# Kernel tuning notes

Hardware: AMD Instinct MI355X
Metric: run time of the kernel (lower is better)

Reference implementation:

```python
import jax, jax.numpy as jnp
import numpy as np

N, D = 1024, 8          # total neurons, neuron_size
I, O = 64, 64           # input / output layer sizes
HN = N - I - O          # hidden layer size (896)
TICKS = 2
DIN = 2 * D + 1         # GRU input: [pre, post, reward]


def setup_inputs() -> dict:
    key = jax.random.key(0)
    ks = jax.random.split(key, 40)

    def rn(k, shape, s=1.0):
        return jax.random.normal(k, shape, jnp.float32) * s

    # Bernoulli(0.5) adjacency + structural validation (as in vallidate_Adjacency_matrix)
    A = np.array(jax.random.uniform(ks[2], (N, N)) < 0.5, dtype=np.int32)
    A[:I, :I] = 0
    A[:I, N - O:] = 0
    A[I:I + HN, :I] = 0
    A[N - O:, :I] = 0
    A[N - O:, N - O:] = 0
    if A[:I].sum() == 0:
        A[0, I] = 1

    inp = {
        'obs': rn(ks[0], (I,)),
        'reward': rn(ks[1], (1,)),
        'adjacency': jnp.asarray(A),
        'hidden0': rn(ks[3], (N, N, D)),
        'post0': rn(ks[4], (N, D)),
        'lr': jnp.full((1,), 0.01, jnp.float32),
    }
    s = 1.0 / np.sqrt(D)
    i = 5
    for pre in ('fc_in', 'fc_hid', 'fc_out'):
        inp[pre + '_w'] = rn(ks[i], (D, D), s); i += 1
        inp[pre + '_b'] = rn(ks[i], (D,), s); i += 1
    for pre in ('gin', 'ghid', 'gout'):
        inp[pre + '_wih'] = rn(ks[i], (3 * D, DIN), s); i += 1
        inp[pre + '_whh'] = rn(ks[i], (3 * D, D), s); i += 1
        inp[pre + '_bih'] = rn(ks[i], (3 * D,), s); i += 1
        inp[pre + '_bhh'] = rn(ks[i], (3 * D,), s); i += 1
    return inp


def _gru(x, h, wih, whh, bih, bhh):
    # torch.nn.GRUCell math
    gx = x @ wih.T + bih          # (..., 3D)
    gh = h @ whh.T + bhh
    xr, xz, xn = jnp.split(gx, 3, axis=-1)
    hr, hz, hn = jnp.split(gh, 3, axis=-1)
    r = jax.nn.sigmoid(xr + hr)
    z = jax.nn.sigmoid(xz + hz)
    n = jnp.tanh(xn + r * hn)
    return (1.0 - z) * n + z * h


def _forward(obs, reward, adjacency, hidden0, post0, lr,
             fc_in_w, fc_in_b, fc_hid_w, fc_hid_b, fc_out_w, fc_out_b,
             gin_wih, gin_whh, gin_bih, gin_bhh,
             ghid_wih, ghid_whh, ghid_bih, ghid_bhh,
             gout_wih, gout_whh, gout_bih, gout_bhh):
    def syn(pre_rows, P, H_read, wih, whh, bih, bhh):
        # dense-masked edge update over an (L, N) layer slice; same math as the
        # per-edge GRUCell, computed for all pairs then masked on write.
        L = pre_rows.shape[0]
        pre = jnp.broadcast_to(pre_rows[:, None, :], (L, N, D))
        post = jnp.broadcast_to(P[None, :, :], (L, N, D))
        rew = jnp.broadcast_to(reward.reshape(1, 1, 1), (L, N, 1))
        x = jnp.concatenate([pre, post, rew], axis=-1)   # (L, N, 2D+1)
        g = _gru(x, H_read, wih, whh, bih, bhh)
        upd = H_read + g * lr
        return upd * pre, upd

    m_in = (adjacency[:I] == 1)[..., None]           # (I, N, 1)
    m_hid = (adjacency[I:I + HN] == 1)[..., None]    # (HN, N, 1)
    m_out = (adjacency[N - O:] == 1)[..., None]      # (O, N, 1)

    inp_sig = jnp.broadcast_to(obs[:, None], (I, D))
    H, P = hidden0, post0
    PH = jnp.zeros((N, N, D), jnp.float32)           # placeholder (persists across ticks)

    for _ in range(TICKS):
        # input layer neurons + synapses (writes rows [:I])
        P = P.at[:I].set(jnp.tanh(inp_sig @ fc_in_w.T + fc_in_b))
        out, upd = syn(P[:I], P, H[:I], gin_wih, gin_whh, gin_bih, gin_bhh)
        PH = PH.at[:I].set(jnp.where(m_in, out, PH[:I]))
        H = H.at[:I].set(jnp.where(m_in, upd, H[:I]))

        # hidden layer neurons + synapses
        P = P.at[I:I + HN].set(jnp.tanh(PH[:, I:I + HN].sum(axis=0) @ fc_hid_w.T + fc_hid_b))
        out, upd = syn(P[I:I + HN], P, H[I:I + HN], ghid_wih, ghid_whh, ghid_bih, ghid_bhh)
        # NOTE: the torch code reads hidden rows offset by I but WRITES unshifted
        # rows [:HN] of both placeholder and hidden_state; replicated faithfully.
        PH = PH.at[:HN].set(jnp.where(m_hid, out, PH[:HN]))
        H = H.at[:HN].set(jnp.where(m_hid, upd, H[:HN]))

        # output layer neurons + synapses
        P = P.at[N - O:].set(jnp.tanh(PH[:, N - O:].sum(axis=0) @ fc_out_w.T + fc_out_b))
        out, upd = syn(P[N - O:], P, H[I + HN:], gout_wih, gout_whh, gout_bih, gout_bhh)
        # torch reads hidden rows offset by I+HN but writes unshifted rows [:O]
        PH = PH.at[:O].set(jnp.where(m_out, out, PH[:O]))
        H = H.at[:O].set(jnp.where(m_out, upd, H[:O]))

    return P


def reference(obs, reward, adjacency, hidden0, post0, lr,
              fc_in_w, fc_in_b, fc_hid_w, fc_hid_b, fc_out_w, fc_out_b,
              gin_wih, gin_whh, gin_bih, gin_bhh,
              ghid_wih, ghid_whh, ghid_bih, ghid_bhh,
              gout_wih, gout_whh, gout_bih, gout_bhh):
    P = _forward(obs, reward, adjacency, hidden0, post0, lr,
                 fc_in_w, fc_in_b, fc_hid_w, fc_hid_b, fc_out_w, fc_out_b,
                 gin_wih, gin_whh, gin_bih, gin_bhh,
                 ghid_wih, ghid_whh, ghid_bih, ghid_bhh,
                 gout_wih, gout_whh, gout_bih, gout_bhh)
    return jnp.argmax(P[N - O:, 0])
```

## Files before the change

kernel.cpp:

```cpp
#include <hip/hip_runtime.h>

#define NN 1024

typedef float f32x8 __attribute__((ext_vector_type(8)));


__device__ __forceinline__ float sigmoid_f(float x)
{
    return __fdividef(1.f, 1.f + __expf(-x));
}
__device__ __forceinline__ float tanh_f(float x)
{
    float ax = fabsf(x);
    float e  = __expf(-2.f * ax);
    float t  = __fdividef(1.f - e, 1.f + e);
    return copysignf(t, x);
}
__device__ __forceinline__ f32x8 ld8(const float* __restrict__ p) { return *(const f32x8*)p; }
__device__ __forceinline__ void st8(float* __restrict__ p, f32x8 v) { *(f32x8*)p = v; }

__device__ __forceinline__ f32x8 gru_core(const float (*__restrict__ sWH)[8],
                                          const float* __restrict__ sGX,
                                          const float* __restrict__ sBhh,
                                          const float* __restrict__ gxp,
                                          f32x8 h, float lr)
{
    f32x8 gr = ld8(gxp), gz = ld8(gxp + 8), gn = ld8(gxp + 16);
    f32x8 upd;
#pragma unroll
    for (int d = 0; d < 8; ++d) {
        float hr = sBhh[d], hz = sBhh[8 + d], hn = sBhh[16 + d];
#pragma unroll
        for (int k = 0; k < 8; ++k) {
            hr = fmaf(sWH[d][k],      h[k], hr);
            hz = fmaf(sWH[8 + d][k],  h[k], hz);
            hn = fmaf(sWH[16 + d][k], h[k], hn);
        }
        float r  = sigmoid_f(sGX[d] + gr[d] + hr);
        float z  = sigmoid_f(sGX[8 + d] + gz[d] + hz);
        float nv = tanh_f(fmaf(r, hn, sGX[16 + d] + gn[d]));
        float g  = (1.f - z) * nv + z * h[d];
        upd[d] = fmaf(g, lr, h[d]);
    }
    return upd;
}

#define SYN_STAGE(PREROW)                                                               \
    __shared__ float sWH[24][8]; __shared__ float sGX[24]; __shared__ float sBhh[24];   \
    { int t_ = threadIdx.x;                                                             \
      if (t_ < 192) { int j = t_ >> 3, k = t_ & 7; sWH[j][k] = Whh[j * 8 + k]; }        \
      else if (t_ < 216) { int j = t_ - 192;                                            \
        float a = Bih[j] + Wih[j * 17 + 16] * reward[0];                                \
        _Pragma("unroll") for (int k = 0; k < 8; ++k)                                   \
            a = fmaf(Wih[j * 17 + k], P[(PREROW) * 8 + k], a);                          \
        sGX[j] = a; sBhh[j] = Bhh[j]; }                                                 \
      __syncthreads(); }

__global__ void __launch_bounds__(256)
k_prep(const float* __restrict__ obs, const float* __restrict__ fiw,
       const float* __restrict__ fib, const float* __restrict__ post0,
       float* __restrict__ P, float* __restrict__ GXPin1, float* __restrict__ GXPhid1,
       const float* __restrict__ gin_wih, const float* __restrict__ ghid_wih)
{
    int t = threadIdx.x, b = blockIdx.x;
    int gid = b * 256 + t;
    float pv;
    if (gid < 512) {
        int i = gid >> 3, j = gid & 7;
        float rs = 0.f;
#pragma unroll
        for (int d = 0; d < 8; ++d) rs += fiw[j * 8 + d];
        pv = tanhf(obs[i] * rs + fib[j]);
    } else {
        pv = post0[gid];
    }
    P[gid] = pv;
    __shared__ float sP[256];
    sP[t] = pv;
    __syncthreads();
    int c0 = b * 32;
    const float* W = nullptr; float* dst = nullptr;
    if (c0 >= 64 && c0 < 960) { W = gin_wih;  dst = GXPin1; }
    else if (c0 >= 960)       { W = ghid_wih; dst = GXPhid1; }
    if (dst) {
        for (int v = t; v < 768; v += 256) {
            int c = v / 24, j = v % 24;
            float a = 0.f;
#pragma unroll
            for (int k = 0; k < 8; ++k) a = fmaf(W[j * 17 + 8 + k], sP[c * 8 + k], a);
            dst[(c0 + c) * 24 + j] = a;
        }
    }
}

template <int TICK>
__global__ void __launch_bounds__(256, 4)
k_syn_in(const int* __restrict__ A, const float* __restrict__ hidden0,
         const float* __restrict__ P, float* __restrict__ PH,
         float* __restrict__ Uin, const float* __restrict__ Utop,
         const float* __restrict__ Uout, const float* __restrict__ GXP,
         const float* __restrict__ Wih, const float* __restrict__ Whh,
         const float* __restrict__ Bih, const float* __restrict__ Bhh,
         const float* __restrict__ reward, const float* __restrict__ lr)
{
    int r = blockIdx.x >> 2;
    SYN_STAGE(r);
    int n = 64 + ((blockIdx.x & 3) << 8) + threadIdx.x;
    if (n >= NN) return;
    int e = (r * NN + n) * 8;
    if (!A[r * NN + n]) {
        if (TICK == 1) { f32x8 z{}; st8(PH + e, z); }
        return;
    }
    f32x8 h;
    if (TICK == 1) {
        h = ld8(hidden0 + e);
    } else {
        const float* src = Uin + e;
        if (A[(960 + r) * NN + n])     src = Uout + e;
        else if (A[(64 + r) * NN + n]) src = Utop + e;
        h = ld8(src);
    }
    f32x8 upd = gru_core(sWH, sGX, sBhh, GXP + n * 24, h, lr[0]);
    f32x8 pre = ld8(P + r * 8);
    st8(PH + e, upd * pre);
    if (TICK == 1) st8(Uin + e, upd);
}

__global__ void __launch_bounds__(256, 4)
k_syn_hid1(const int* __restrict__ A, const float* __restrict__ hidden0,
           const float* __restrict__ P, float* __restrict__ PH,
           float* __restrict__ Utop, float* __restrict__ Urt,
           const float* __restrict__ GXP,
           const float* __restrict__ Wih, const float* __restrict__ Whh,
           const float* __restrict__ Bih, const float* __restrict__ Bhh,
           const float* __restrict__ reward, const float* __restrict__ lr)
{
    int l = blockIdx.x >> 2;
    SYN_STAGE(64 + l);
    int n = 64 + ((blockIdx.x & 3) << 8) + threadIdx.x;
    if (n >= NN) return;
    int e = (l * NN + n) * 8;
    if (!A[(64 + l) * NN + n]) {
        if (l >= 64) { f32x8 z{}; st8(PH + e, z); }
        return;
    }
    f32x8 h = ld8(hidden0 + ((64 + l) * NN + n) * 8);
    f32x8 upd = gru_core(sWH, sGX, sBhh, GXP + n * 24, h, lr[0]);
    f32x8 pre = ld8(P + (64 + l) * 8);
    st8(PH + e, upd * pre);
    if (l < 64) st8(Utop + e, upd);
    if (n >= 960) st8(Urt + (l * 64 + (n - 960)) * 8, upd);
}

__global__ void __launch_bounds__(256, 4)
k_syn_out(const int* __restrict__ A, const float* __restrict__ hidden0,
          const float* __restrict__ P, float* __restrict__ PH,
          float* __restrict__ Uout, const float* __restrict__ GXP,
          const float* __restrict__ Wih, const float* __restrict__ Whh,
          const float* __restrict__ Bih, const float* __restrict__ Bhh,
          const float* __restrict__ reward, const float* __restrict__ lr)
{
    int l = blockIdx.x >> 2;
    SYN_STAGE(960 + l);
    int n = 64 + ((blockIdx.x & 3) << 8) + threadIdx.x;
    if (n >= NN) return;
    if (!A[(960 + l) * NN + n]) return;
    f32x8 h = ld8(hidden0 + ((960 + l) * NN + n) * 8);
    f32x8 upd = gru_core(sWH, sGX, sBhh, GXP + n * 24, h, lr[0]);
    f32x8 pre = ld8(P + (960 + l) * 8);
    int e = (l * NN + n) * 8;
    st8(PH + e, upd * pre);
    st8(Uout + e, upd);
}

__global__ void __launch_bounds__(256, 4)
k_syn_hid2(const int* __restrict__ A, const float* __restrict__ hidden0,
           const float* __restrict__ P, float* __restrict__ PH,
           const float* __restrict__ Urt, const float* __restrict__ GXP,
           const float* __restrict__ Wih, const float* __restrict__ Whh,
           const float* __restrict__ Bih, const float* __restrict__ Bhh,
           const float* __restrict__ reward, const float* __restrict__ lr)
{
    __shared__ float sWH[24][8]; __shared__ float sBhh[24]; __shared__ float sGX4[4][24];
    int t = threadIdx.x;
    if (t < 192) { int j = t >> 3, k = t & 7; sWH[j][k] = Whh[j * 8 + k]; }
    else if (t < 216) sBhh[t - 192] = Bhh[t - 192];
    if (t < 96) {
        int rr = t / 24, j = t % 24;
        int l = blockIdx.x * 4 + rr;
        float a = Bih[j] + Wih[j * 17 + 16] * reward[0];
#pragma unroll
        for (int k = 0; k < 8; ++k) a = fmaf(Wih[j * 17 + k], P[(64 + l) * 8 + k], a);
        sGX4[rr][j] = a;
    }
    __syncthreads();
    int rr = t >> 6, nn = t & 63;
    int l = blockIdx.x * 4 + rr, n = 960 + nn;
    if (!A[(64 + l) * NN + n]) return;
    const float* hp = (l < 832 && A[(128 + l) * NN + n]) ? (Urt + ((64 + l) * 64 + nn) * 8)
                                                         : (hidden0 + ((64 + l) * NN + n) * 8);
    f32x8 h = ld8(hp);
    f32x8 upd = gru_core(sWH, sGX4[rr], sBhh, GXP + n * 24, h, lr[0]);
    f32x8 pre = ld8(P + (64 + l) * 8);
    st8(PH + (l * NN + n) * 8, upd * pre);
}

__global__ void __launch_bounds__(256)
k_sum_hid1(const float* __restrict__ PH, float* __restrict__ P,
           const float* __restrict__ W, const float* __restrict__ b,
           float* __restrict__ GXPhid1, float* __restrict__ GXPout,
           float* __restrict__ GXPin2,
           const float* __restrict__ ghid_wih, const float* __restrict__ gout_wih,
           const float* __restrict__ gin_wih)
{
    int t = threadIdx.x;
    int c0 = 64 + blockIdx.x * 32;
    int base = c0 * 8 + t;
    float acc = 0.f;
    for (int r = 0; r < 64; ++r) acc += PH[r * 8192 + base];
    __shared__ float sS[256];
    sS[t] = acc; __syncthreads();
    int j = t & 7;
    float z = b[j];
#pragma unroll
    for (int d = 0; d < 8; ++d) z = fmaf(sS[(t & ~7) | d], W[j * 8 + d], z);
    float pv = tanhf(z);
    P[base] = pv;
    __shared__ float sP[256];
    sP[t] = pv; __syncthreads();
    for (int v = t; v < 768; v += 256) {
        int c = v / 24, jj = v % 24;
        float a1 = 0.f, a2 = 0.f, a3 = 0.f;
#pragma unroll
        for (int k = 0; k < 8; ++k) {
            float p = sP[c * 8 + k];
            a1 = fmaf(ghid_wih[jj * 17 + 8 + k], p, a1);
            a2 = fmaf(gout_wih[jj * 17 + 8 + k], p, a2);
            a3 = fmaf(gin_wih [jj * 17 + 8 + k], p, a3);
        }
        int o = (c0 + c) * 24 + jj;
        GXPhid1[o] = a1; GXPout[o] = a2; GXPin2[o] = a3;
    }
}

template <bool DO_GXP>
__global__ void __launch_bounds__(512)
k_sumN(const float* __restrict__ PH, float* __restrict__ P,
       const float* __restrict__ W, const float* __restrict__ b,
       int col0, float* __restrict__ GXPdst, const float* __restrict__ gWih)
{
    int t = threadIdx.x;
    int col = (t >> 3) & 7, dim = t & 7, chunk = t >> 6;
    int gc0 = col0 + blockIdx.x * 8;
    float acc = 0.f;
    int base = (gc0 + col) * 8 + dim;
    for (int r = chunk * 112; r < chunk * 112 + 112; ++r) acc += PH[r * 8192 + base];
    __shared__ float sA[8][64];
    sA[chunk][(col << 3) | dim] = acc;
    __syncthreads();
    __shared__ float sS[64];
    if (t < 64) {
        float s = 0.f;
#pragma unroll
        for (int c = 0; c < 8; ++c) s += sA[c][t];
        sS[t] = s;
    }
    __syncthreads();
    __shared__ float sPn[64];
    if (t < 64) {
        int cl = t >> 3, j = t & 7;
        float z = b[j];
#pragma unroll
        for (int d = 0; d < 8; ++d) z = fmaf(sS[(cl << 3) | d], W[j * 8 + d], z);
        float pv = tanhf(z);
        P[(gc0 + cl) * 8 + j] = pv;
        sPn[t] = pv;
    }
    __syncthreads();
    if (DO_GXP && t < 192) {
        int c = t / 24, j = t % 24;
        float a = 0.f;
#pragma unroll
        for (int k = 0; k < 8; ++k) a = fmaf(gWih[j * 17 + 8 + k], sPn[c * 8 + k], a);
        GXPdst[(gc0 + c) * 24 + j] = a;
    }
}

__global__ void __launch_bounds__(64)
k_argmax(const float* __restrict__ P, float* __restrict__ out)
{
    __shared__ float v[64];
    int t = threadIdx.x;
    v[t] = P[(960 + t) * 8];
    __syncthreads();
    if (t == 0) {
        int best = 0; float bv = v[0];
        for (int j = 1; j < 64; ++j)
            if (v[j] > bv) { bv = v[j]; best = j; }
        out[0] = (float)best;
    }
}

extern "C" void kernel_launch(void* const* d_in, const int* in_sizes, int n_in,
                              void* d_out, int out_size, void* d_ws, size_t ws_size,
                              hipStream_t stream)
{
    const float* obs      = (const float*)d_in[0];
    const float* reward   = (const float*)d_in[1];
    const int*   A        = (const int*)d_in[2];
    const float* hidden0  = (const float*)d_in[3];
    const float* post0    = (const float*)d_in[4];
    const float* lr       = (const float*)d_in[5];
    const float* fc_in_w  = (const float*)d_in[6];
    const float* fc_in_b  = (const float*)d_in[7];
    const float* fc_hid_w = (const float*)d_in[8];
    const float* fc_hid_b = (const float*)d_in[9];
    const float* fc_out_w = (const float*)d_in[10];
    const float* fc_out_b = (const float*)d_in[11];
    const float* gin_wih  = (const float*)d_in[12];
    const float* gin_whh  = (const float*)d_in[13];
    const float* gin_bih  = (const float*)d_in[14];
    const float* gin_bhh  = (const float*)d_in[15];
    const float* ghid_wih = (const float*)d_in[16];
    const float* ghid_whh = (const float*)d_in[17];
    const float* ghid_bih = (const float*)d_in[18];
    const float* ghid_bhh = (const float*)d_in[19];
    const float* gout_wih = (const float*)d_in[20];
    const float* gout_whh = (const float*)d_in[21];
    const float* gout_bih = (const float*)d_in[22];
    const float* gout_bhh = (const float*)d_in[23];

    float* ws      = (float*)d_ws;
    float* PH      = ws;
    float* Uin     = ws + 7340032;
    float* Utop    = Uin + 524288;
    float* Urt     = Utop + 524288;
    float* Uout    = Urt + 458752;
    float* P       = Uout + 524288;
    float* GXPin1  = P + 8192;
    float* GXPhid1 = GXPin1 + 24576;
    float* GXPout  = GXPhid1 + 24576;
    float* GXPin2  = GXPout + 24576;
    float* GXPhid2 = GXPin2 + 24576;

    k_prep<<<32, 256, 0, stream>>>(obs, fc_in_w, fc_in_b, post0, P,
                                   GXPin1, GXPhid1, gin_wih, ghid_wih);

    k_syn_in<1><<<256, 256, 0, stream>>>(A, hidden0, P, PH, Uin, Utop, Uout, GXPin1,
                                         gin_wih, gin_whh, gin_bih, gin_bhh, reward, lr);
    k_sum_hid1<<<28, 256, 0, stream>>>(PH, P, fc_hid_w, fc_hid_b,
                                       GXPhid1, GXPout, GXPin2,
                                       ghid_wih, gout_wih, gin_wih);
    k_syn_hid1<<<3584, 256, 0, stream>>>(A, hidden0, P, PH, Utop, Urt, GXPhid1,
                                         ghid_wih, ghid_whh, ghid_bih, ghid_bhh, reward, lr);
    k_sumN<true><<<8, 512, 0, stream>>>(PH, P, fc_out_w, fc_out_b, 960, GXPhid2, ghid_wih);
    k_syn_out<<<256, 256, 0, stream>>>(A, hidden0, P, PH, Uout, GXPout,
                                       gout_wih, gout_whh, gout_bih, gout_bhh, reward, lr);

    k_syn_in<2><<<256, 256, 0, stream>>>(A, hidden0, P, PH, Uin, Utop, Uout, GXPin2,
                                         gin_wih, gin_whh, gin_bih, gin_bhh, reward, lr);
    k_sumN<false><<<112, 512, 0, stream>>>(PH, P, fc_hid_w, fc_hid_b, 64, nullptr, nullptr);
    k_syn_hid2<<<224, 256, 0, stream>>>(A, hidden0, P, PH, Urt, GXPhid2,
                                        ghid_wih, ghid_whh, ghid_bih, ghid_bhh, reward, lr);
    k_sumN<false><<<8, 512, 0, stream>>>(PH, P, fc_out_w, fc_out_b, 960, nullptr, nullptr);

    k_argmax<<<1, 64, 0, stream>>>(P, (float*)d_out);
}
```

Before: 76.28 us.

## Retile hidden synapse kernel and fuse column partial sums to skip PH writes

The tick-1 hidden synapse kernel is retiled into 64-column by 16-row blocks. Each thread now handles four rows and reuses its GX projections across them. Column partial sums are reduced in shared memory and written to a small Spart buffer, so hidden rows 64+ no longer store the full PH tensor except for the output columns. A new k_sum_hid2 reads the first 64 PH rows plus the partial sums instead of scanning the whole 896-row PH slab. This cuts large global writes and reads, at the cost of fewer blocks and an extra block-level sync and reduction.

```diff
diff --git a/kernel.cpp b/kernel.cpp
--- a/kernel.cpp
+++ b/kernel.cpp
@@ -22,10 +22,9 @@
 __device__ __forceinline__ f32x8 gru_core(const float (*__restrict__ sWH)[8],
                                           const float* __restrict__ sGX,
                                           const float* __restrict__ sBhh,
-                                          const float* __restrict__ gxp,
+                                          f32x8 gr, f32x8 gz, f32x8 gn,
                                           f32x8 h, float lr)
 {
-    f32x8 gr = ld8(gxp), gz = ld8(gxp + 8), gn = ld8(gxp + 16);
     f32x8 upd;
 #pragma unroll
     for (int d = 0; d < 8; ++d) {
@@ -121,7 +120,8 @@
         else if (A[(64 + r) * NN + n]) src = Utop + e;
         h = ld8(src);
     }
-    f32x8 upd = gru_core(sWH, sGX, sBhh, GXP + n * 24, h, lr[0]);
+    const float* gxp = GXP + n * 24;
+    f32x8 upd = gru_core(sWH, sGX, sBhh, ld8(gxp), ld8(gxp + 8), ld8(gxp + 16), h, lr[0]);
     f32x8 pre = ld8(P + r * 8);
     st8(PH + e, upd * pre);
     if (TICK == 1) st8(Uin + e, upd);
@@ -131,26 +131,68 @@
 k_syn_hid1(const int* __restrict__ A, const float* __restrict__ hidden0,
            const float* __restrict__ P, float* __restrict__ PH,
            float* __restrict__ Utop, float* __restrict__ Urt,
-           const float* __restrict__ GXP,
+           float* __restrict__ Spart, const float* __restrict__ GXP,
            const float* __restrict__ Wih, const float* __restrict__ Whh,
            const float* __restrict__ Bih, const float* __restrict__ Bhh,
            const float* __restrict__ reward, const float* __restrict__ lr)
 {
-    int l = blockIdx.x >> 2;
-    SYN_STAGE(64 + l);
-    int n = 64 + ((blockIdx.x & 3) << 8) + threadIdx.x;
-    if (n >= NN) return;
-    int e = (l * NN + n) * 8;
-    if (!A[(64 + l) * NN + n]) {
-        if (l >= 64) { f32x8 z{}; st8(PH + e, z); }
-        return;
-    }
-    f32x8 h = ld8(hidden0 + ((64 + l) * NN + n) * 8);
-    f32x8 upd = gru_core(sWH, sGX, sBhh, GXP + n * 24, h, lr[0]);
-    f32x8 pre = ld8(P + (64 + l) * 8);
-    st8(PH + e, upd * pre);
-    if (l < 64) st8(Utop + e, upd);
-    if (n >= 960) st8(Urt + (l * 64 + (n - 960)) * 8, upd);
+    int ct = blockIdx.x, rt = blockIdx.y;
+    int cbase = 64 + ct * 64;
+    __shared__ float sWH[24][8];
+    __shared__ float sBhh[24];
+    __shared__ __align__(32) float sGX[16][24];
+    __shared__ __align__(32) float sPre[16][8];
+    int t = threadIdx.x;
+    if (t < 192) { int j = t >> 3, k = t & 7; sWH[j][k] = Whh[j * 8 + k]; }
+    else if (t < 216) sBhh[t - 192] = Bhh[t - 192];
+    if (t < 128) { int rr = t >> 3, k = t & 7; sPre[rr][k] = P[(64 + rt * 16 + rr) * 8 + k]; }
+    for (int v = t; v < 384; v += 256) {
+        int rr = v / 24, j = v % 24;
+        float a = Bih[j] + Wih[j * 17 + 16] * reward[0];
+#pragma unroll
+        for (int k = 0; k < 8; ++k)
+            a = fmaf(Wih[j * 17 + k], P[(64 + rt * 16 + rr) * 8 + k], a);
+        sGX[rr][j] = a;
+    }
+    __syncthreads();
+    int cc = t & 63, rg = t >> 6;
+    int n = cbase + cc;
+    const float* gxp = GXP + n * 24;
+    f32x8 gr = ld8(gxp), gz = ld8(gxp + 8), gn = ld8(gxp + 16);
+    float lrv = lr[0];
+    f32x8 acc{};
+#pragma unroll
+    for (int rr2 = 0; rr2 < 4; ++rr2) {
+        int rr = rg * 4 + rr2;
+        int l = rt * 16 + rr;
+        int e = (l * NN + n) * 8;
+        bool act = A[(64 + l) * NN + n] != 0;
+        f32x8 out{};
+        if (act) {
+            f32x8 h = ld8(hidden0 + ((64 + l) * NN + n) * 8);
+            f32x8 upd = gru_core(sWH, sGX[rr], sBhh, gr, gz, gn, h, lrv);
+            f32x8 pre = ld8(&sPre[rr][0]);
+            out = upd * pre;
+            if (l < 64) { st8(PH + e, out); st8(Utop + e, upd); }
+            else if (ct == 14) st8(PH + e, out);
+            if (ct == 14) st8(Urt + (l * 64 + cc) * 8, upd);
+        } else if (ct == 14 && l >= 64) {
+            st8(PH + e, out);
+        }
+        acc += out;
+    }
+    if (ct < 14) {
+        __shared__ float sRed[4][64][8];
+        st8(&sRed[rg][cc][0], acc);
+        __syncthreads();
+        if (rt >= 4) {
+            for (int v = t; v < 512; v += 256) {
+                int col = v >> 3, d = v & 7;
+                float s = sRed[0][col][d] + sRed[1][col][d] + sRed[2][col][d] + sRed[3][col][d];
+                Spart[(rt * 896 + (cbase - 64) + col) * 8 + d] = s;
+            }
+        }
+    }
 }
 
 __global__ void __launch_bounds__(256, 4)
@@ -167,7 +209,8 @@
     if (n >= NN) return;
     if (!A[(960 + l) * NN + n]) return;
     f32x8 h = ld8(hidden0 + ((960 + l) * NN + n) * 8);
-    f32x8 upd = gru_core(sWH, sGX, sBhh, GXP + n * 24, h, lr[0]);
+    const float* gxp = GXP + n * 24;
+    f32x8 upd = gru_core(sWH, sGX, sBhh, ld8(gxp), ld8(gxp + 8), ld8(gxp + 16), h, lr[0]);
     f32x8 pre = ld8(P + (960 + l) * 8);
     int e = (l * NN + n) * 8;
     st8(PH + e, upd * pre);
@@ -201,7 +244,8 @@
     const float* hp = (l < 832 && A[(128 + l) * NN + n]) ? (Urt + ((64 + l) * 64 + nn) * 8)
                                                          : (hidden0 + ((64 + l) * NN + n) * 8);
     f32x8 h = ld8(hp);
-    f32x8 upd = gru_core(sWH, sGX4[rr], sBhh, GXP + n * 24, h, lr[0]);
+    const float* gxp = GXP + n * 24;
+    f32x8 upd = gru_core(sWH, sGX4[rr], sBhh, ld8(gxp), ld8(gxp + 8), ld8(gxp + 16), h, lr[0]);
     f32x8 pre = ld8(P + (64 + l) * 8);
     st8(PH + (l * NN + n) * 8, upd * pre);
 }
@@ -242,6 +286,27 @@
         int o = (c0 + c) * 24 + jj;
         GXPhid1[o] = a1; GXPout[o] = a2; GXPin2[o] = a3;
     }
+}
+
+__global__ void __launch_bounds__(256)
+k_sum_hid2(const float* __restrict__ PH, const float* __restrict__ Spart,
+           float* __restrict__ P, const float* __restrict__ W,
+           const float* __restrict__ b)
+{
+    int t = threadIdx.x;
+    int c0 = 64 + blockIdx.x * 32;
+    int base = c0 * 8 + t;
+    float acc = 0.f;
+    for (int r = 0; r < 64; ++r) acc += PH[r * 8192 + base];
+    const float* sp = Spart + (c0 - 64) * 8 + t;
+    for (int rt = 4; rt < 56; ++rt) acc += sp[rt * 7168];
+    __shared__ float sS[256];
+    sS[t] = acc; __syncthreads();
+    int j = t & 7;
+    float z = b[j];
+#pragma unroll
+    for (int d = 0; d < 8; ++d) z = fmaf(sS[(t & ~7) | d], W[j * 8 + d], z);
+    P[base] = tanhf(z);
 }
 
 template <bool DO_GXP>
@@ -343,6 +408,7 @@
     float* GXPout  = GXPhid1 + 24576;
     float* GXPin2  = GXPout + 24576;
     float* GXPhid2 = GXPin2 + 24576;
+    float* Spart   = GXPhid2 + 24576;
 
     k_prep<<<32, 256, 0, stream>>>(obs, fc_in_w, fc_in_b, post0, P,
                                    GXPin1, GXPhid1, gin_wih, ghid_wih);
@@ -352,15 +418,16 @@
     k_sum_hid1<<<28, 256, 0, stream>>>(PH, P, fc_hid_w, fc_hid_b,
                                        GXPhid1, GXPout, GXPin2,
                                        ghid_wih, gout_wih, gin_wih);
-    k_syn_hid1<<<3584, 256, 0, stream>>>(A, hidden0, P, PH, Utop, Urt, GXPhid1,
-                                         ghid_wih, ghid_whh, ghid_bih, ghid_bhh, reward, lr);
+    k_syn_hid1<<<dim3(15, 56), 256, 0, stream>>>(A, hidden0, P, PH, Utop, Urt, Spart,
+                                                 GXPhid1, ghid_wih, ghid_whh, ghid_bih,
+                                                 ghid_bhh, reward, lr);
     k_sumN<true><<<8, 512, 0, stream>>>(PH, P, fc_out_w, fc_out_b, 960, GXPhid2, ghid_wih);
     k_syn_out<<<256, 256, 0, stream>>>(A, hidden0, P, PH, Uout, GXPout,
                                        gout_wih, gout_whh, gout_bih, gout_bhh, reward, lr);
 
     k_syn_in<2><<<256, 256, 0, stream>>>(A, hidden0, P, PH, Uin, Utop, Uout, GXPin2,
                                          gin_wih, gin_whh, gin_bih, gin_bhh, reward, lr);
-    k_sumN<false><<<112, 512, 0, stream>>>(PH, P, fc_hid_w, fc_hid_b, 64, nullptr, nullptr);
+    k_sum_hid2<<<28, 256, 0, stream>>>(PH, Spart, P, fc_hid_w, fc_hid_b);
     k_syn_hid2<<<224, 256, 0, stream>>>(A, hidden0, P, PH, Urt, GXPhid2,
                                         ghid_wih, ghid_whh, ghid_bih, ghid_bhh, reward, lr);
     k_sumN<false><<<8, 512, 0, stream>>>(PH, P, fc_out_w, fc_out_b, 960, nullptr, nullptr);
```

New measurement: 117.6 us. +54.1%, slower.

## Accumulate hidden-layer column sums via atomics instead of storing and re-reading PH

Applied to the files above, without the earlier changes.

In the hidden synapse stage, rows beyond the first 64 that target hidden columns no longer write their products to the large PH buffer. Each thread instead atomically adds them into a small column-sum buffer T, which the prep kernel zeroes. A new k_sum_hid2 kernel then reads only the 64 overwritten PH rows plus T, replacing the tick-2 hidden reduction over 896 rows. The aim is to cut heavy PH write and read traffic, at the cost of contended float atomics and a nondeterministic summation order. The output-column reduction is also reshaped to 16 blocks of 256 threads.

```diff
diff --git a/kernel.cpp b/kernel.cpp
--- a/kernel.cpp
+++ b/kernel.cpp
@@ -22,10 +22,9 @@
 __device__ __forceinline__ f32x8 gru_core(const float (*__restrict__ sWH)[8],
                                           const float* __restrict__ sGX,
                                           const float* __restrict__ sBhh,
-                                          const float* __restrict__ gxp,
+                                          f32x8 gr, f32x8 gz, f32x8 gn,
                                           f32x8 h, float lr)
 {
-    f32x8 gr = ld8(gxp), gz = ld8(gxp + 8), gn = ld8(gxp + 16);
     f32x8 upd;
 #pragma unroll
     for (int d = 0; d < 8; ++d) {
@@ -59,11 +58,13 @@
 __global__ void __launch_bounds__(256)
 k_prep(const float* __restrict__ obs, const float* __restrict__ fiw,
        const float* __restrict__ fib, const float* __restrict__ post0,
-       float* __restrict__ P, float* __restrict__ GXPin1, float* __restrict__ GXPhid1,
+       float* __restrict__ P, float* __restrict__ T,
+       float* __restrict__ GXPin1, float* __restrict__ GXPhid1,
        const float* __restrict__ gin_wih, const float* __restrict__ ghid_wih)
 {
     int t = threadIdx.x, b = blockIdx.x;
     int gid = b * 256 + t;
+    if (gid < 7168) T[gid] = 0.f;
     float pv;
     if (gid < 512) {
         int i = gid >> 3, j = gid & 7;
@@ -121,7 +122,8 @@
         else if (A[(64 + r) * NN + n]) src = Utop + e;
         h = ld8(src);
     }
-    f32x8 upd = gru_core(sWH, sGX, sBhh, GXP + n * 24, h, lr[0]);
+    const float* gxp = GXP + n * 24;
+    f32x8 upd = gru_core(sWH, sGX, sBhh, ld8(gxp), ld8(gxp + 8), ld8(gxp + 16), h, lr[0]);
     f32x8 pre = ld8(P + r * 8);
     st8(PH + e, upd * pre);
     if (TICK == 1) st8(Uin + e, upd);
@@ -131,7 +133,7 @@
 k_syn_hid1(const int* __restrict__ A, const float* __restrict__ hidden0,
            const float* __restrict__ P, float* __restrict__ PH,
            float* __restrict__ Utop, float* __restrict__ Urt,
-           const float* __restrict__ GXP,
+           float* __restrict__ T, const float* __restrict__ GXP,
            const float* __restrict__ Wih, const float* __restrict__ Whh,
            const float* __restrict__ Bih, const float* __restrict__ Bhh,
            const float* __restrict__ reward, const float* __restrict__ lr)
@@ -142,15 +144,22 @@
     if (n >= NN) return;
     int e = (l * NN + n) * 8;
     if (!A[(64 + l) * NN + n]) {
-        if (l >= 64) { f32x8 z{}; st8(PH + e, z); }
+        if (l >= 64 && n >= 960) { f32x8 z{}; st8(PH + e, z); }
         return;
     }
     f32x8 h = ld8(hidden0 + ((64 + l) * NN + n) * 8);
-    f32x8 upd = gru_core(sWH, sGX, sBhh, GXP + n * 24, h, lr[0]);
+    const float* gxp = GXP + n * 24;
+    f32x8 upd = gru_core(sWH, sGX, sBhh, ld8(gxp), ld8(gxp + 8), ld8(gxp + 16), h, lr[0]);
     f32x8 pre = ld8(P + (64 + l) * 8);
-    st8(PH + e, upd * pre);
-    if (l < 64) st8(Utop + e, upd);
+    f32x8 out = upd * pre;
+    if (l < 64) { st8(PH + e, out); st8(Utop + e, upd); }
+    else if (n >= 960) st8(PH + e, out);
     if (n >= 960) st8(Urt + (l * 64 + (n - 960)) * 8, upd);
+    if (l >= 64 && n < 960) {
+        float* tp = T + (n - 64) * 8;
+#pragma unroll
+        for (int d = 0; d < 8; ++d) atomicAdd(tp + d, out[d]);
+    }
 }
 
 __global__ void __launch_bounds__(256, 4)
@@ -167,7 +176,8 @@
     if (n >= NN) return;
     if (!A[(960 + l) * NN + n]) return;
     f32x8 h = ld8(hidden0 + ((960 + l) * NN + n) * 8);
-    f32x8 upd = gru_core(sWH, sGX, sBhh, GXP + n * 24, h, lr[0]);
+    const float* gxp = GXP + n * 24;
+    f32x8 upd = gru_core(sWH, sGX, sBhh, ld8(gxp), ld8(gxp + 8), ld8(gxp + 16), h, lr[0]);
     f32x8 pre = ld8(P + (960 + l) * 8);
     int e = (l * NN + n) * 8;
     st8(PH + e, upd * pre);
@@ -201,7 +211,8 @@
     const float* hp = (l < 832 && A[(128 + l) * NN + n]) ? (Urt + ((64 + l) * 64 + nn) * 8)
                                                          : (hidden0 + ((64 + l) * NN + n) * 8);
     f32x8 h = ld8(hp);
-    f32x8 upd = gru_core(sWH, sGX4[rr], sBhh, GXP + n * 24, h, lr[0]);
+    const float* gxp = GXP + n * 24;
+    f32x8 upd = gru_core(sWH, sGX4[rr], sBhh, ld8(gxp), ld8(gxp + 8), ld8(gxp + 16), h, lr[0]);
     f32x8 pre = ld8(P + (64 + l) * 8);
     st8(PH + (l * NN + n) * 8, upd * pre);
 }
@@ -244,31 +255,50 @@
     }
 }
 
+__global__ void __launch_bounds__(256)
+k_sum_hid2(const float* __restrict__ PH, const float* __restrict__ T,
+           float* __restrict__ P, const float* __restrict__ W,
+           const float* __restrict__ b)
+{
+    int t = threadIdx.x;
+    int c0 = 64 + blockIdx.x * 32;
+    int base = c0 * 8 + t;
+    float acc = T[(c0 - 64) * 8 + t];
+    for (int r = 0; r < 64; ++r) acc += PH[r * 8192 + base];
+    __shared__ float sS[256];
+    sS[t] = acc; __syncthreads();
+    int j = t & 7;
+    float z = b[j];
+#pragma unroll
+    for (int d = 0; d < 8; ++d) z = fmaf(sS[(t & ~7) | d], W[j * 8 + d], z);
+    P[base] = tanhf(z);
+}
+
 template <bool DO_GXP>
-__global__ void __launch_bounds__(512)
+__global__ void __launch_bounds__(256)
 k_sumN(const float* __restrict__ PH, float* __restrict__ P,
        const float* __restrict__ W, const float* __restrict__ b,
-       int col0, float* __restrict__ GXPdst, const float* __restrict__ gWih)
+       float* __restrict__ GXPdst, const float* __restrict__ gWih)
 {
     int t = threadIdx.x;
-    int col = (t >> 3) & 7, dim = t & 7, chunk = t >> 6;
-    int gc0 = col0 + blockIdx.x * 8;
+    int chunk = t >> 5, col = (t >> 3) & 3, dim = t & 7;
+    int gc0 = 960 + blockIdx.x * 4;
     float acc = 0.f;
     int base = (gc0 + col) * 8 + dim;
     for (int r = chunk * 112; r < chunk * 112 + 112; ++r) acc += PH[r * 8192 + base];
-    __shared__ float sA[8][64];
+    __shared__ float sA[8][32];
     sA[chunk][(col << 3) | dim] = acc;
     __syncthreads();
-    __shared__ float sS[64];
-    if (t < 64) {
+    __shared__ float sS[32];
+    if (t < 32) {
         float s = 0.f;
 #pragma unroll
         for (int c = 0; c < 8; ++c) s += sA[c][t];
         sS[t] = s;
     }
     __syncthreads();
-    __shared__ float sPn[64];
-    if (t < 64) {
+    __shared__ float sPn[32];
+    if (t < 32) {
         int cl = t >> 3, j = t & 7;
         float z = b[j];
 #pragma unroll
@@ -278,7 +308,7 @@
         sPn[t] = pv;
     }
     __syncthreads();
-    if (DO_GXP && t < 192) {
+    if (DO_GXP && t < 96) {
         int c = t / 24, j = t % 24;
         float a = 0.f;
 #pragma unroll
@@ -343,8 +373,9 @@
     float* GXPout  = GXPhid1 + 24576;
     float* GXPin2  = GXPout + 24576;
     float* GXPhid2 = GXPin2 + 24576;
-
-    k_prep<<<32, 256, 0, stream>>>(obs, fc_in_w, fc_in_b, post0, P,
+    float* T       = GXPhid2 + 24576;
+
+    k_prep<<<32, 256, 0, stream>>>(obs, fc_in_w, fc_in_b, post0, P, T,
                                    GXPin1, GXPhid1, gin_wih, ghid_wih);
 
     k_syn_in<1><<<256, 256, 0, stream>>>(A, hidden0, P, PH, Uin, Utop, Uout, GXPin1,
@@ -352,18 +383,18 @@
     k_sum_hid1<<<28, 256, 0, stream>>>(PH, P, fc_hid_w, fc_hid_b,
                                        GXPhid1, GXPout, GXPin2,
                                        ghid_wih, gout_wih, gin_wih);
-    k_syn_hid1<<<3584, 256, 0, stream>>>(A, hidden0, P, PH, Utop, Urt, GXPhid1,
+    k_syn_hid1<<<3584, 256, 0, stream>>>(A, hidden0, P, PH, Utop, Urt, T, GXPhid1,
                                          ghid_wih, ghid_whh, ghid_bih, ghid_bhh, reward, lr);
-    k_sumN<true><<<8, 512, 0, stream>>>(PH, P, fc_out_w, fc_out_b, 960, GXPhid2, ghid_wih);
+    k_sumN<true><<<16, 256, 0, stream>>>(PH, P, fc_out_w, fc_out_b, GXPhid2, ghid_wih);
     k_syn_out<<<256, 256, 0, stream>>>(A, hidden0, P, PH, Uout, GXPout,
                                        gout_wih, gout_whh, gout_bih, gout_bhh, reward, lr);
 
     k_syn_in<2><<<256, 256, 0, stream>>>(A, hidden0, P, PH, Uin, Utop, Uout, GXPin2,
                                          gin_wih, gin_whh, gin_bih, gin_bhh, reward, lr);
-    k_sumN<false><<<112, 512, 0, stream>>>(PH, P, fc_hid_w, fc_hid_b, 64, nullptr, nullptr);
+    k_sum_hid2<<<28, 256, 0, stream>>>(PH, T, P, fc_hid_w, fc_hid_b);
     k_syn_hid2<<<224, 256, 0, stream>>>(A, hidden0, P, PH, Urt, GXPhid2,
                                         ghid_wih, ghid_whh, ghid_bih, ghid_bhh, reward, lr);
-    k_sumN<false><<<8, 512, 0, stream>>>(PH, P, fc_out_w, fc_out_b, 960, nullptr, nullptr);
+    k_sumN<false><<<16, 256, 0, stream>>>(PH, P, fc_out_w, fc_out_b, nullptr, nullptr);
 
     k_argmax<<<1, 64, 0, stream>>>(P, (float*)d_out);
 }
```

After: 188.3 us. 147% more time.
